# Kernel tuning notes

Hardware: AMD Instinct MI355X
Metric: run time of the kernel (lower is better)

## Reference

```python
import jax, jax.numpy as jnp
import numpy as np
import math

B, SQ, SK, DQ, DK, DV = 8, 1024, 1024, 512, 512, 512


def setup_inputs() -> dict:
    key = jax.random.key(0)
    ks = jax.random.split(key, 12)
    s = lambda fan_in: 1.0 / math.sqrt(fan_in)
    return {
        "Q": jax.random.normal(ks[0], (B, SQ, DQ), jnp.float32),
        "K": jax.random.normal(ks[1], (B, SK, DK), jnp.float32),
        "Wq": jax.random.uniform(ks[2], (DV, DQ), jnp.float32, -s(DQ), s(DQ)),
        "bq": jax.random.uniform(ks[3], (DV,), jnp.float32, -s(DQ), s(DQ)),
        "Wk": jax.random.uniform(ks[4], (DV, DK), jnp.float32, -s(DK), s(DK)),
        "bk": jax.random.uniform(ks[5], (DV,), jnp.float32, -s(DK), s(DK)),
        "Wv": jax.random.uniform(ks[6], (DV, DK), jnp.float32, -s(DK), s(DK)),
        "bv": jax.random.uniform(ks[7], (DV,), jnp.float32, -s(DK), s(DK)),
        "Wo": jax.random.uniform(ks[8], (DV, DV), jnp.float32, -s(DV), s(DV)),
        "bo": jax.random.uniform(ks[9], (DV,), jnp.float32, -s(DV), s(DV)),
        "num_heads": 8,
    }


def reference(Q, K, Wq, bq, Wk, bk, Wv, bv, Wo, bo, num_heads):
    dim_V = Wq.shape[0]
    dh = dim_V // num_heads
    b, sq, _ = Q.shape
    sk = K.shape[1]
    # projections (torch Linear: x @ W.T + b)
    Qp = Q @ Wq.T + bq                      # [B, Sq, Dv]
    Kp = K @ Wk.T + bk                      # [B, Sk, Dv]
    Vp = K @ Wv.T + bv                      # [B, Sk, Dv]
    # manual head split (split along feature, cat along batch) == reshape to heads
    Qh = Qp.reshape(b, sq, num_heads, dh)   # [B, Sq, H, dh]
    Kh = Kp.reshape(b, sk, num_heads, dh)
    Vh = Vp.reshape(b, sk, num_heads, dh)
    # NOTE: scale is sqrt(dim_V), not sqrt(head_dim), as in the source.
    scores = jnp.einsum("bqhd,bkhd->bhqk", Qh, Kh) / jnp.sqrt(
        jnp.asarray(dim_V, Qh.dtype))
    A = jax.nn.softmax(scores, axis=-1)     # [B, H, Sq, Sk]
    ctx = jnp.einsum("bhqk,bkhd->bqhd", A, Vh)
    O = (Qh + ctx).reshape(b, sq, dim_V)    # residual on projected Q, merge heads
    O = O + jax.nn.relu(O @ Wo.T + bo)      # FFN residual
    return O
```

## Files before the change

### kernel.cpp

```cpp
#include <hip/hip_runtime.h>

typedef unsigned short u16;
typedef __attribute__((ext_vector_type(8))) short short8;
typedef __attribute__((ext_vector_type(4))) float f32x4;
typedef __attribute__((ext_vector_type(2))) unsigned uint2v;

__device__ __forceinline__ u16 f2bf(float f) {
  union { float f; unsigned u; } v; v.f = f;
  unsigned r = v.u + 0x7FFFu + ((v.u >> 16) & 1u);
  return (u16)(r >> 16);
}
__device__ __forceinline__ float bf2f(u16 u) {
  union { unsigned u; float f; } v; v.u = ((unsigned)u) << 16;
  return v.f;
}
__device__ __forceinline__ void gload_lds16(const u16* g, u16* l) {
  __builtin_amdgcn_global_load_lds((const __attribute__((address_space(1))) void*)g,
                                   (__attribute__((address_space(3))) void*)l,
                                   16, 0, 0);
}
__device__ __forceinline__ void gload_lds16f(const float* g, u16* l) {
  __builtin_amdgcn_global_load_lds((const __attribute__((address_space(1))) void*)g,
                                   (__attribute__((address_space(3))) void*)l,
                                   16, 0, 0);
}

#if __has_builtin(__builtin_amdgcn_exp2f)
#define EXP2(x) __builtin_amdgcn_exp2f(x)
#else
#define EXP2(x) exp2f(x)
#endif

#define BATCH 8
#define SEQ   1024
#define DIM   512
#define NH    8
#define DH    64
#define MROWS (BATCH * SEQ)

__global__ void cvt_w(const float* __restrict__ Wq, const float* __restrict__ Wk,
                      const float* __restrict__ Wv, const float* __restrict__ Wo,
                      u16* __restrict__ out) {
  const float* s = (blockIdx.y == 0) ? Wq : (blockIdx.y == 1) ? Wk
                   : (blockIdx.y == 2) ? Wv : Wo;
  const float4* src = (const float4*)s;
  u16* dst = out + (size_t)blockIdx.y * (DIM * DIM);
  int i = blockIdx.x * 256 + threadIdx.x;
  float4 v = src[i];
  ushort4 r;
  r.x = f2bf(v.x); r.y = f2bf(v.y); r.z = f2bf(v.z); r.w = f2bf(v.w);
  *(ushort4*)&dst[i * 4] = r;
}

__global__ __launch_bounds__(256, 3) void proj_gemm(
    const float* __restrict__ Qf, const float* __restrict__ Kf,
    const u16* __restrict__ Wbf,
    const float* __restrict__ bq, const float* __restrict__ bk,
    const float* __restrict__ bv,
    u16* __restrict__ Qp, u16* __restrict__ Kp, u16* __restrict__ VpT) {
  __shared__ alignas(16) u16 ldsA[2 * 8192];
  __shared__ alignas(16) u16 ldsB[2 * 4096];

  const int tid = threadIdx.x;
  const int z = blockIdx.z;
  const int m0 = blockIdx.x * 128;
  const int n0 = blockIdx.y * 128;

  const float* A32 = (z == 0) ? Qf : Kf;
  const u16* W = Wbf + (size_t)z * (DIM * DIM);
  const float* bias = (z == 0) ? bq : (z == 1) ? bk : bv;

  const int lane = tid & 63;
  const int wv = tid >> 6;
  const int wr = wv >> 1, wc = wv & 1;
  const int lr = lane & 15, lg = lane >> 4;
  const int wbase = tid & 192;

  const int schunk = (tid & 7) ^ ((tid >> 3) & 7);
  const float* abase = A32 + (size_t)(m0 + (tid >> 3)) * DIM + schunk * 4;

#define PSTAGE_A(buf, kt)                                                       \
  {                                                                             \
    _Pragma("unroll")                                                           \
    for (int i = 0; i < 4; ++i) {                                               \
      gload_lds16f(abase + (size_t)(i * 32) * DIM + (kt) * 32,                  \
                   ldsA + (buf) * 8192 + (i * 256 + wbase) * 8);                \
    }                                                                           \
  }

#define PSTAGE_B(buf, kt)                                                       \
  {                                                                             \
    _Pragma("unroll")                                                           \
    for (int i = 0; i < 2; ++i) {                                               \
      const int T = i * 256 + tid;                                              \
      const int row = T & 127, kc = T >> 7;                                     \
      gload_lds16(W + (size_t)(n0 + row) * DIM + (kt) * 32 + kc * 8,            \
                  ldsB + (buf) * 4096 + (i * 256 + wbase) * 8);                 \
    }                                                                           \
  }

  const int xr = lr & 7;
  const int aoff0 = (wr * 64 + lr) * 64 + (((2 * lg) ^ xr) * 8);
  const int aoff1 = (wr * 64 + lr) * 64 + (((2 * lg + 1) ^ xr) * 8);

  f32x4 acc[4][4] = {};

  PSTAGE_A(0, 0);
  PSTAGE_B(0, 0);
  __syncthreads();

  int cur = 0;
#pragma unroll 1
  for (int kt = 0; kt < 16; ++kt) {
    if (kt < 15) { PSTAGE_A(cur ^ 1, kt + 1); PSTAGE_B(cur ^ 1, kt + 1); }

    short8 av[4], bw[4];
#pragma unroll
    for (int m = 0; m < 4; ++m) {
      f32x4 a0 = *(const f32x4*)(ldsA + cur * 8192 + aoff0 + m * 16 * 64);
      f32x4 a1 = *(const f32x4*)(ldsA + cur * 8192 + aoff1 + m * 16 * 64);
      unsigned u0, u1, u2, u3;
      asm("v_cvt_pk_bf16_f32 %0, %1, %2" : "=v"(u0) : "v"(a0[0]), "v"(a0[1]));
      asm("v_cvt_pk_bf16_f32 %0, %1, %2" : "=v"(u1) : "v"(a0[2]), "v"(a0[3]));
      asm("v_cvt_pk_bf16_f32 %0, %1, %2" : "=v"(u2) : "v"(a1[0]), "v"(a1[1]));
      asm("v_cvt_pk_bf16_f32 %0, %1, %2" : "=v"(u3) : "v"(a1[2]), "v"(a1[3]));
      union { unsigned u[4]; short8 s; } pk_;
      pk_.u[0] = u0; pk_.u[1] = u1; pk_.u[2] = u2; pk_.u[3] = u3;
      av[m] = pk_.s;
    }
#pragma unroll
    for (int n = 0; n < 4; ++n)
      bw[n] = *(const short8*)(ldsB + cur * 4096 + (lg * 128 + wc * 64 + n * 16 + lr) * 8);
#pragma unroll
    for (int m = 0; m < 4; ++m)
#pragma unroll
      for (int n = 0; n < 4; ++n)
        acc[m][n] = __builtin_amdgcn_mfma_f32_16x16x32_bf16(av[m], bw[n], acc[m][n], 0, 0, 0);
    __syncthreads();
    cur ^= 1;
  }
#undef PSTAGE_A
#undef PSTAGE_B

  float bn[4];
#pragma unroll
  for (int n = 0; n < 4; ++n) bn[n] = bias[n0 + wc * 64 + n * 16 + lr];

  if (z < 2) {
    u16* outp = (z == 0) ? Qp : Kp;
#pragma unroll
    for (int m = 0; m < 4; ++m)
#pragma unroll
      for (int n = 0; n < 4; ++n)
#pragma unroll
        for (int r = 0; r < 4; ++r) {
          const int row = m0 + wr * 64 + m * 16 + lg * 4 + r;
          const int col = n0 + wc * 64 + n * 16 + lr;
          outp[(size_t)row * DIM + col] = f2bf(acc[m][n][r] + bn[n]);
        }
  } else {
#pragma unroll
    for (int m = 0; m < 4; ++m)
#pragma unroll
      for (int n = 0; n < 4; ++n) {
        const int grow = m0 + wr * 64 + m * 16 + lg * 4;
        const int b = grow >> 10;
        const int s = grow & 1023;
        const int col = n0 + wc * 64 + n * 16 + lr;
        ushort4 pk;
        pk.x = f2bf(acc[m][n][0] + bn[n]);
        pk.y = f2bf(acc[m][n][1] + bn[n]);
        pk.z = f2bf(acc[m][n][2] + bn[n]);
        pk.w = f2bf(acc[m][n][3] + bn[n]);
        *(ushort4*)&VpT[(size_t)b * (DIM * SEQ) + (size_t)col * SEQ + s] = pk;
      }
  }
}

__global__ __launch_bounds__(512, 4) void attn_kernel(
    const u16* __restrict__ Qp, const u16* __restrict__ Kp,
    const u16* __restrict__ VpT, u16* __restrict__ Opre) {
  __shared__ alignas(16) u16 klds[2][4096];
  __shared__ alignas(16) u16 vlds[2][4096];
  __shared__ alignas(16) u16 plds[8][64 * 16];

  const int tid = threadIdx.x;
  const int lane = tid & 63, wv = tid >> 6;
  const int lr = lane & 15, lg = lane >> 4;
  const int q0 = blockIdx.y * 128;
  const int b = blockIdx.x >> 3, h = blockIdx.x & 7;
  const size_t rowbase = (size_t)b * SEQ;
  const int hoff = h * DH;

  const float csc = 0.063762f;
  short8 aq[2];
#pragma unroll
  for (int t = 0; t < 2; ++t) {
    short8 raw = *(const short8*)(Qp + (rowbase + q0 + wv * 16 + lr) * DIM +
                                  hoff + t * 32 + lg * 8);
    short8 s;
#pragma unroll
    for (int j = 0; j < 8; ++j) s[j] = (short)f2bf(bf2f((u16)raw[j]) * csc);
    aq[t] = s;
  }

  short8 ones;
#pragma unroll
  for (int j = 0; j < 8; ++j) ones[j] = (short)0x3F80;

#define STAGEKV(buf, kt)                                                        \
  {                                                                             \
    const int ks0_ = (kt) * 64;                                                 \
    const int rr = tid & 63, cc = tid >> 6;                                     \
    const int srr = rr ^ (cc << 1);                                             \
    gload_lds16(Kp + (rowbase + ks0_ + srr) * DIM + hoff + cc * 8,              \
                &klds[buf][tid * 8]);                                           \
    gload_lds16(VpT + (size_t)b * (DIM * SEQ) + (size_t)(hoff + srr) * SEQ +    \
                    ks0_ + cc * 8,                                              \
                &vlds[buf][tid * 8]);                                           \
  }

  const int kx0 = lr ^ (lg << 1);

  u16* pw = &plds[wv][0];
  unsigned pbase = (unsigned)(uintptr_t)(__attribute__((address_space(3))) u16*)pw;
  const unsigned ta00 = pbase + (unsigned)lg * 128u;
  const unsigned ta01 = ta00 + 128u;
  const unsigned ta10 = ta00 + 1024u;
  const unsigned ta11 = ta00 + 1152u;

  f32x4 l_acc = {};
  f32x4 o_acc[4] = {};

  STAGEKV(0, 0);
  __syncthreads();

  int cur = 0;
#pragma unroll 1
  for (int kt = 0; kt < 16; ++kt) {
    if (kt < 15) STAGEKV(cur ^ 1, kt + 1);

    f32x4 sa[4] = {};
    __builtin_amdgcn_s_setprio(1);
#pragma unroll
    for (int t = 0; t < 2; ++t) {
      const int kxt = kx0 ^ (t << 3);
#pragma unroll
      for (int f = 0; f < 4; ++f) {
        short8 bk_ = *(const short8*)(&klds[cur][((lg + 4 * t) * 64 + f * 16 + kxt) * 8]);
        sa[f] = __builtin_amdgcn_mfma_f32_16x16x32_bf16(aq[t], bk_, sa[f], 0, 0, 0);
      }
    }
    __builtin_amdgcn_s_setprio(0);

    short8 bvf[8];
#pragma unroll
    for (int n = 0; n < 4; ++n)
#pragma unroll
      for (int t = 0; t < 2; ++t) {
        const int kxt = kx0 ^ (t << 3);
        bvf[n * 2 + t] = *(const short8*)(&vlds[cur][((lg + 4 * t) * 64 + n * 16 + kxt) * 8]);
      }

#pragma unroll
    for (int f = 0; f < 4; ++f) {
      float p0 = EXP2(sa[f][0]);
      float p1 = EXP2(sa[f][1]);
      float p2 = EXP2(sa[f][2]);
      float p3 = EXP2(sa[f][3]);
      unsigned lo, hi;
      asm("v_cvt_pk_bf16_f32 %0, %1, %2" : "=v"(lo) : "v"(p0), "v"(p1));
      asm("v_cvt_pk_bf16_f32 %0, %1, %2" : "=v"(hi) : "v"(p2), "v"(p3));
      uint2v pk; pk.x = lo; pk.y = hi;
      *(uint2v*)&pw[(f * 16 + lr) * 16 + lg * 4] = pk;
    }

    asm volatile("s_waitcnt lgkmcnt(0)" ::: "memory");
    uint2v t00, t01, t10, t11;
    asm volatile("ds_read_b64_tr_b16 %0, %1" : "=v"(t00) : "v"(ta00));
    asm volatile("ds_read_b64_tr_b16 %0, %1" : "=v"(t01) : "v"(ta01));
    asm volatile("ds_read_b64_tr_b16 %0, %1" : "=v"(t10) : "v"(ta10));
    asm volatile("ds_read_b64_tr_b16 %0, %1" : "=v"(t11) : "v"(ta11));
    asm volatile("s_waitcnt lgkmcnt(0)" ::: "memory");
    __builtin_amdgcn_sched_barrier(0);

    short8 ap[2];
    {
      union { unsigned u[4]; short8 s; } u0, u1;
      u0.u[0] = t00.x; u0.u[1] = t00.y; u0.u[2] = t01.x; u0.u[3] = t01.y;
      u1.u[0] = t10.x; u1.u[1] = t10.y; u1.u[2] = t11.x; u1.u[3] = t11.y;
      ap[0] = u0.s; ap[1] = u1.s;
    }

    __builtin_amdgcn_s_setprio(1);
#pragma unroll
    for (int n = 0; n < 4; ++n)
#pragma unroll
      for (int t = 0; t < 2; ++t)
        o_acc[n] = __builtin_amdgcn_mfma_f32_16x16x32_bf16(ap[t], bvf[n * 2 + t], o_acc[n], 0, 0, 0);
    l_acc = __builtin_amdgcn_mfma_f32_16x16x32_bf16(ap[0], ones, l_acc, 0, 0, 0);
    l_acc = __builtin_amdgcn_mfma_f32_16x16x32_bf16(ap[1], ones, l_acc, 0, 0, 0);
    __builtin_amdgcn_s_setprio(0);

    __syncthreads();
    cur ^= 1;
  }
#undef STAGEKV

  float inv[4];
#pragma unroll
  for (int r = 0; r < 4; ++r) inv[r] = 1.0f / l_acc[r];
#pragma unroll
  for (int n = 0; n < 4; ++n)
#pragma unroll
    for (int r = 0; r < 4; ++r) {
      const size_t row = rowbase + q0 + wv * 16 + lg * 4 + r;
      const int col = hoff + n * 16 + lr;
      const float ctx = o_acc[n][r] * inv[r];
      const float qv = bf2f(Qp[row * DIM + col]);
      Opre[row * DIM + col] = f2bf(qv + ctx);
    }
}

__global__ __launch_bounds__(256, 4) void ffn_gemm(
    const u16* __restrict__ Opre, const u16* __restrict__ Wo_bf,
    const float* __restrict__ bo, float* __restrict__ out) {
  __shared__ alignas(16) u16 ldsA[2 * 2048];
  __shared__ alignas(16) u16 ldsB[2 * 4096];

  const int tid = threadIdx.x;
  const int m0 = blockIdx.x * 64;
  const int n0 = blockIdx.y * 128;

  const int lane = tid & 63;
  const int wv = tid >> 6;
  const int wr = wv >> 1, wc = wv & 1;
  const int lr = lane & 15, lg = lane >> 4;
  const int wbase = tid & 192;

#define FSTAGE(buf, kt)                                                         \
  {                                                                             \
    const int rr = tid & 63, cc = tid >> 6;                                     \
    gload_lds16(Opre + (size_t)(m0 + rr) * DIM + (kt) * 32 + cc * 8,            \
                ldsA + (buf) * 2048 + tid * 8);                                 \
    _Pragma("unroll")                                                           \
    for (int i = 0; i < 2; ++i) {                                               \
      const int T = i * 256 + tid;                                              \
      const int row = T & 127, kc = T >> 7;                                     \
      gload_lds16(Wo_bf + (size_t)(n0 + row) * DIM + (kt) * 32 + kc * 8,        \
                  ldsB + (buf) * 4096 + (i * 256 + wbase) * 8);                 \
    }                                                                           \
  }

  f32x4 acc[2][4] = {};

  FSTAGE(0, 0);
  __syncthreads();

  int cur = 0;
#pragma unroll 1
  for (int kt = 0; kt < 16; ++kt) {
    if (kt < 15) FSTAGE(cur ^ 1, kt + 1);
    short8 av[2], bw[4];
#pragma unroll
    for (int m = 0; m < 2; ++m)
      av[m] = *(const short8*)(ldsA + cur * 2048 + (lg * 64 + wr * 32 + m * 16 + lr) * 8);
#pragma unroll
    for (int n = 0; n < 4; ++n)
      bw[n] = *(const short8*)(ldsB + cur * 4096 + (lg * 128 + wc * 64 + n * 16 + lr) * 8);
#pragma unroll
    for (int m = 0; m < 2; ++m)
#pragma unroll
      for (int n = 0; n < 4; ++n)
        acc[m][n] = __builtin_amdgcn_mfma_f32_16x16x32_bf16(av[m], bw[n], acc[m][n], 0, 0, 0);
    __syncthreads();
    cur ^= 1;
  }
#undef FSTAGE

  float bn[4];
#pragma unroll
  for (int n = 0; n < 4; ++n) bn[n] = bo[n0 + wc * 64 + n * 16 + lr];

#pragma unroll
  for (int m = 0; m < 2; ++m)
#pragma unroll
    for (int n = 0; n < 4; ++n)
#pragma unroll
      for (int r = 0; r < 4; ++r) {
        const int row = m0 + wr * 32 + m * 16 + lg * 4 + r;
        const int col = n0 + wc * 64 + n * 16 + lr;
        const float v = acc[m][n][r] + bn[n];
        const float o = bf2f(Opre[(size_t)row * DIM + col]);
        out[(size_t)row * DIM + col] = o + fmaxf(v, 0.f);
      }
}

extern "C" void kernel_launch(void* const* d_in, const int* in_sizes, int n_in,
                              void* d_out, int out_size, void* d_ws, size_t ws_size,
                              hipStream_t stream) {
  const float* Q  = (const float*)d_in[0];
  const float* K  = (const float*)d_in[1];
  const float* Wq = (const float*)d_in[2];
  const float* bq = (const float*)d_in[3];
  const float* Wk = (const float*)d_in[4];
  const float* bk = (const float*)d_in[5];
  const float* Wv = (const float*)d_in[6];
  const float* bv = (const float*)d_in[7];
  const float* Wo = (const float*)d_in[8];
  const float* bo = (const float*)d_in[9];

  char* ws = (char*)d_ws;
  const size_t SZ = (size_t)MROWS * DIM * sizeof(u16);
  const size_t WSZ = 4 * (size_t)(DIM * DIM) * sizeof(u16);
  u16* Wbf  = (u16*)(ws + 0);
  u16* Qp   = (u16*)(ws + WSZ);
  u16* Kp   = (u16*)((char*)Qp + SZ);
  u16* VpT  = (u16*)((char*)Kp + SZ);
  u16* Opre = (u16*)((char*)VpT + SZ);

  cvt_w<<<dim3(256, 4), 256, 0, stream>>>(Wq, Wk, Wv, Wo, Wbf);
  proj_gemm<<<dim3(64, 4, 3), 256, 0, stream>>>(Q, K, Wbf, bq, bk, bv, Qp, Kp, VpT);
  attn_kernel<<<dim3(64, 8), 512, 0, stream>>>(Qp, Kp, VpT, Opre);
  ffn_gemm<<<dim3(128, 4), 256, 0, stream>>>(Opre, Wbf + 3 * (DIM * DIM), bo, (float*)d_out);
}
```

Measured before the change: 80.82 us.

## Stage fp32 A tiles through registers, convert to bf16 before LDS write

```diff
diff --git a/kernel.cpp b/kernel.cpp
--- a/kernel.cpp
+++ b/kernel.cpp
@@ -15,11 +15,6 @@
   return v.f;
 }
 __device__ __forceinline__ void gload_lds16(const u16* g, u16* l) {
-  __builtin_amdgcn_global_load_lds((const __attribute__((address_space(1))) void*)g,
-                                   (__attribute__((address_space(3))) void*)l,
-                                   16, 0, 0);
-}
-__device__ __forceinline__ void gload_lds16f(const float* g, u16* l) {
   __builtin_amdgcn_global_load_lds((const __attribute__((address_space(1))) void*)g,
                                    (__attribute__((address_space(3))) void*)l,
                                    16, 0, 0);
@@ -37,6 +32,9 @@
 #define NH    8
 #define DH    64
 #define MROWS (BATCH * SEQ)
+
+#define ASTRIDE 1040
+#define ABUF    (4 * ASTRIDE)
 
 __global__ void cvt_w(const float* __restrict__ Wq, const float* __restrict__ Wk,
                       const float* __restrict__ Wv, const float* __restrict__ Wo,
@@ -52,13 +50,13 @@
   *(ushort4*)&dst[i * 4] = r;
 }
 
-__global__ __launch_bounds__(256, 3) void proj_gemm(
+__global__ __launch_bounds__(256, 4) void proj_gemm(
     const float* __restrict__ Qf, const float* __restrict__ Kf,
     const u16* __restrict__ Wbf,
     const float* __restrict__ bq, const float* __restrict__ bk,
     const float* __restrict__ bv,
     u16* __restrict__ Qp, u16* __restrict__ Kp, u16* __restrict__ VpT) {
-  __shared__ alignas(16) u16 ldsA[2 * 8192];
+  __shared__ alignas(16) u16 ldsA[2 * ABUF];
   __shared__ alignas(16) u16 ldsB[2 * 4096];
 
   const int tid = threadIdx.x;
@@ -76,15 +74,17 @@
   const int lr = lane & 15, lg = lane >> 4;
   const int wbase = tid & 192;
 
-  const int schunk = (tid & 7) ^ ((tid >> 3) & 7);
-  const float* abase = A32 + (size_t)(m0 + (tid >> 3)) * DIM + schunk * 4;
-
-#define PSTAGE_A(buf, kt)                                                       \
+  float4 fA[2][2];
+
+#define PISSUE_A(kt)                                                            \
   {                                                                             \
     _Pragma("unroll")                                                           \
-    for (int i = 0; i < 4; ++i) {                                               \
-      gload_lds16f(abase + (size_t)(i * 32) * DIM + (kt) * 32,                  \
-                   ldsA + (buf) * 8192 + (i * 256 + wbase) * 8);                \
+    for (int i = 0; i < 2; ++i) {                                               \
+      const int T = i * 256 + tid;                                              \
+      const int row = T >> 2, cc = T & 3;                                       \
+      const float* g = A32 + (size_t)(m0 + row) * DIM + (kt) * 32 + cc * 8;     \
+      fA[i][0] = *(const float4*)g;                                             \
+      fA[i][1] = *(const float4*)(g + 4);                                       \
     }                                                                           \
   }
 
@@ -99,35 +99,39 @@
     }                                                                           \
   }
 
-  const int xr = lr & 7;
-  const int aoff0 = (wr * 64 + lr) * 64 + (((2 * lg) ^ xr) * 8);
-  const int aoff1 = (wr * 64 + lr) * 64 + (((2 * lg + 1) ^ xr) * 8);
+#define PWRITE_A(buf)                                                           \
+  {                                                                             \
+    _Pragma("unroll")                                                           \
+    for (int i = 0; i < 2; ++i) {                                               \
+      const int T = i * 256 + tid;                                              \
+      const int row = T >> 2, cc = T & 3;                                       \
+      unsigned w0, w1, w2, w3;                                                  \
+      asm("v_cvt_pk_bf16_f32 %0, %1, %2" : "=v"(w0) : "v"(fA[i][0].x), "v"(fA[i][0].y)); \
+      asm("v_cvt_pk_bf16_f32 %0, %1, %2" : "=v"(w1) : "v"(fA[i][0].z), "v"(fA[i][0].w)); \
+      asm("v_cvt_pk_bf16_f32 %0, %1, %2" : "=v"(w2) : "v"(fA[i][1].x), "v"(fA[i][1].y)); \
+      asm("v_cvt_pk_bf16_f32 %0, %1, %2" : "=v"(w3) : "v"(fA[i][1].z), "v"(fA[i][1].w)); \
+      union { unsigned u[4]; short8 s; } pk_;                                   \
+      pk_.u[0] = w0; pk_.u[1] = w1; pk_.u[2] = w2; pk_.u[3] = w3;               \
+      *(short8*)(ldsA + (buf) * ABUF + cc * ASTRIDE + row * 8) = pk_.s;         \
+    }                                                                           \
+  }
 
   f32x4 acc[4][4] = {};
 
-  PSTAGE_A(0, 0);
+  PISSUE_A(0);
   PSTAGE_B(0, 0);
+  PWRITE_A(0);
   __syncthreads();
 
   int cur = 0;
 #pragma unroll 1
   for (int kt = 0; kt < 16; ++kt) {
-    if (kt < 15) { PSTAGE_A(cur ^ 1, kt + 1); PSTAGE_B(cur ^ 1, kt + 1); }
-
+    if (kt < 15) { PISSUE_A(kt + 1); PSTAGE_B(cur ^ 1, kt + 1); }
     short8 av[4], bw[4];
 #pragma unroll
-    for (int m = 0; m < 4; ++m) {
-      f32x4 a0 = *(const f32x4*)(ldsA + cur * 8192 + aoff0 + m * 16 * 64);
-      f32x4 a1 = *(const f32x4*)(ldsA + cur * 8192 + aoff1 + m * 16 * 64);
-      unsigned u0, u1, u2, u3;
-      asm("v_cvt_pk_bf16_f32 %0, %1, %2" : "=v"(u0) : "v"(a0[0]), "v"(a0[1]));
-      asm("v_cvt_pk_bf16_f32 %0, %1, %2" : "=v"(u1) : "v"(a0[2]), "v"(a0[3]));
-      asm("v_cvt_pk_bf16_f32 %0, %1, %2" : "=v"(u2) : "v"(a1[0]), "v"(a1[1]));
-      asm("v_cvt_pk_bf16_f32 %0, %1, %2" : "=v"(u3) : "v"(a1[2]), "v"(a1[3]));
-      union { unsigned u[4]; short8 s; } pk_;
-      pk_.u[0] = u0; pk_.u[1] = u1; pk_.u[2] = u2; pk_.u[3] = u3;
-      av[m] = pk_.s;
-    }
+    for (int m = 0; m < 4; ++m)
+      av[m] = *(const short8*)(ldsA + cur * ABUF + lg * ASTRIDE +
+                               (wr * 64 + m * 16 + lr) * 8);
 #pragma unroll
     for (int n = 0; n < 4; ++n)
       bw[n] = *(const short8*)(ldsB + cur * 4096 + (lg * 128 + wc * 64 + n * 16 + lr) * 8);
@@ -136,11 +140,13 @@
 #pragma unroll
       for (int n = 0; n < 4; ++n)
         acc[m][n] = __builtin_amdgcn_mfma_f32_16x16x32_bf16(av[m], bw[n], acc[m][n], 0, 0, 0);
+    if (kt < 15) PWRITE_A(cur ^ 1);
     __syncthreads();
     cur ^= 1;
   }
-#undef PSTAGE_A
+#undef PISSUE_A
 #undef PSTAGE_B
+#undef PWRITE_A
 
   float bn[4];
 #pragma unroll
```

Result: no change. 81.08 us (+0.3%).
